# Kernel optimization log

Measured on AMD Instinct MI355X. Metric: run time of the kernel, lower is better.

The kernel has to match this reference:

```python
import jax, jax.numpy as jnp
import numpy as np

ALPHA = 0.2  # LeakyReLU negative slope

def setup_inputs() -> dict:
    key = jax.random.key(0)
    k1, k2, k3, k4 = jax.random.split(key, 4)
    N, F_in, F_out = 8192, 512, 64
    x = jax.random.normal(k1, (N, F_in), dtype=jnp.float32)
    adj = jax.random.randint(k2, (N, N), 0, 2, dtype=jnp.int32)
    # xavier-normal-ish init
    weight = jax.random.normal(k3, (F_in, F_out), dtype=jnp.float32) * np.sqrt(2.0 / (F_in + F_out))
    a = jax.random.normal(k4, (2 * F_out, 1), dtype=jnp.float32) * np.sqrt(2.0 / (2 * F_out + 1))
    return {"x": x, "adj": adj, "weight": weight, "a": a}

def reference(x, adj, weight, a):
    # Wh: [N, F_out]
    Wh = x @ weight
    F_out = weight.shape[1]
    a1 = a[:F_out, 0]   # applies to source (row) node
    a2 = a[F_out:, 0]   # applies to target (col) node
    # e[i,j] = LeakyReLU(Wh[i]@a1 + Wh[j]@a2)  -- broadcast-add instead of O(N^2*2F) concat
    s1 = Wh @ a1        # [N]
    s2 = Wh @ a2        # [N]
    e = s1[:, None] + s2[None, :]              # [N, N]
    e = jnp.where(e > 0, e, ALPHA * e)         # LeakyReLU
    e = jnp.where(adj > 0, e, jnp.float32(-9e15))
    attention = jax.nn.softmax(e, axis=1)      # [N, N]
    h_prime = attention @ Wh                   # [N, F_out]
    return jax.nn.elu(h_prime)                 # concat=True -> ELU
```

## Files before the change

### kernel.cpp

```cpp
#include <hip/hip_runtime.h>
#include <hip/hip_bf16.h>
#include <cstdint>
#include <cstddef>

#define N_NODES 8192
#define F_IN 512
#define F_OUT 64
#define LOG2E 1.44269504f

#define JSPLIT 8
#define JPB (N_NODES / JSPLIT)

typedef __attribute__((ext_vector_type(8))) short short8v;
typedef __attribute__((ext_vector_type(4))) float f32x4;
typedef __attribute__((ext_vector_type(4))) int i32x4;
typedef __attribute__((ext_vector_type(4))) unsigned int u32x4;

static __device__ __forceinline__ unsigned short f2bf(float f) {
    union { float f; unsigned u; } v; v.f = f;
    unsigned u = v.u + 0x7FFFu + ((v.u >> 16) & 1u);
    return (unsigned short)(u >> 16);
}
static __device__ __forceinline__ float bf2f(unsigned short b) {
    union { unsigned u; float f; } v; v.u = ((unsigned)b) << 16;
    return v.f;
}
static __device__ __forceinline__ unsigned cvt_pk_bf16(float lo, float hi) {
    unsigned r;
    asm("v_cvt_pk_bf16_f32 %0, %1, %2" : "=v"(r) : "v"(lo), "v"(hi));
    return r;
}

__global__ __launch_bounds__(256)
void gat_wconv(const float* __restrict__ W, unsigned short* __restrict__ whf,
               unsigned short* __restrict__ wlf) {
    const int t = blockIdx.x * 256 + threadIdx.x;
    const int tile = t >> 6, lane = t & 63;
    const int kt = tile >> 2, ct = tile & 3;
    const int k0 = kt * 32 + ((lane >> 4) << 3);
    const int c  = ct * 16 + (lane & 15);
    short8v h, l;
    #pragma unroll
    for (int i = 0; i < 8; ++i) {
        float v = W[(size_t)(k0 + i) * F_OUT + c];
        unsigned short hb = f2bf(v);
        h[i] = (short)hb;
        l[i] = (short)f2bf(v - bf2f(hb));
    }
    const size_t dst = (size_t)tile * 512 + (size_t)lane * 8;
    *(short8v*)(whf + dst) = h;
    *(short8v*)(wlf + dst) = l;
}

__global__ __launch_bounds__(256)
void gat_prep(const float* __restrict__ x, const unsigned short* __restrict__ whf,
              const unsigned short* __restrict__ wlf, const float* __restrict__ a,
              unsigned short* __restrict__ whtf,
              float* __restrict__ s1, float* __restrict__ s2) {
    __shared__ f32x4 red[2][4][64];
    __shared__ unsigned short ldsT[64][40];
    const int tid = threadIdx.x;
    const int lane = tid & 63;
    const int wv = tid >> 6;
    const int rt = wv & 1;
    const int kh = wv >> 1;
    const int l15 = lane & 15, g = lane >> 4;
    const int jt = blockIdx.x;
    const int row0 = jt * 32 + rt * 16;

    f32x4 acc[4] = {{0.f,0.f,0.f,0.f},{0.f,0.f,0.f,0.f},{0.f,0.f,0.f,0.f},{0.f,0.f,0.f,0.f}};

    const float* xp = x + (size_t)(row0 + l15) * F_IN + kh * 256 + g * 8;
    float4 v[16];
    #pragma unroll
    for (int q = 0; q < 8; ++q) {
        v[2 * q]     = *(const float4*)(xp + q * 32);
        v[2 * q + 1] = *(const float4*)(xp + q * 32 + 4);
    }
    #pragma unroll
    for (int q = 0; q < 8; ++q) {
        const int kt = kh * 8 + q;
        float vv[8] = {v[2*q].x, v[2*q].y, v[2*q].z, v[2*q].w,
                       v[2*q+1].x, v[2*q+1].y, v[2*q+1].z, v[2*q+1].w};
        short8v xh, xl;
        #pragma unroll
        for (int i = 0; i < 8; ++i) {
            unsigned short hb = f2bf(vv[i]);
            xh[i] = (short)hb;
            xl[i] = (short)f2bf(vv[i] - bf2f(hb));
        }
        const unsigned short* wp = whf + (size_t)(kt * 4) * 512 + (size_t)lane * 8;
        const unsigned short* lp = wlf + (size_t)(kt * 4) * 512 + (size_t)lane * 8;
        #pragma unroll
        for (int ct = 0; ct < 4; ++ct) {
            short8v wh = *(const short8v*)(wp + ct * 512);
            short8v wl = *(const short8v*)(lp + ct * 512);
            acc[ct] = __builtin_amdgcn_mfma_f32_16x16x32_bf16(xh, wh, acc[ct], 0, 0, 0);
            acc[ct] = __builtin_amdgcn_mfma_f32_16x16x32_bf16(xl, wh, acc[ct], 0, 0, 0);
            acc[ct] = __builtin_amdgcn_mfma_f32_16x16x32_bf16(xh, wl, acc[ct], 0, 0, 0);
        }
    }

    if (kh == 1) {
        #pragma unroll
        for (int ct = 0; ct < 4; ++ct) red[rt][ct][lane] = acc[ct];
    }
    __syncthreads();

    if (kh == 0) {
        #pragma unroll
        for (int ct = 0; ct < 4; ++ct) acc[ct] += red[rt][ct][lane];

        #pragma unroll
        for (int r = 0; r < 4; ++r) {
            float p1 = 0.f, p2 = 0.f;
            #pragma unroll
            for (int ct = 0; ct < 4; ++ct) {
                p1 = fmaf(acc[ct][r], a[ct * 16 + l15], p1);
                p2 = fmaf(acc[ct][r], a[64 + ct * 16 + l15], p2);
            }
            p1 += __shfl_xor(p1, 1); p2 += __shfl_xor(p2, 1);
            p1 += __shfl_xor(p1, 2); p2 += __shfl_xor(p2, 2);
            p1 += __shfl_xor(p1, 4); p2 += __shfl_xor(p2, 4);
            p1 += __shfl_xor(p1, 8); p2 += __shfl_xor(p2, 8);
            if (l15 == 0) {
                s1[row0 + g * 4 + r] = p1 * LOG2E;
                s2[row0 + g * 4 + r] = p2 * LOG2E;
            }
        }

        #pragma unroll
        for (int ct = 0; ct < 4; ++ct) {
            ushort4 pk;
            pk.x = f2bf(acc[ct][0]); pk.y = f2bf(acc[ct][1]);
            pk.z = f2bf(acc[ct][2]); pk.w = f2bf(acc[ct][3]);
            *(ushort4*)&ldsT[ct * 16 + l15][rt * 16 + g * 4] = pk;
        }
    }
    __syncthreads();

    if (kh == 0) {
        #pragma unroll
        for (int fl = 0; fl < 2; ++fl) {
            const int ft = rt * 2 + fl;
            short8v sv = *(const short8v*)&ldsT[ft * 16 + l15][g * 8];
            *(short8v*)(whtf + ((size_t)jt * 4 + ft) * 512 + (size_t)lane * 8) = sv;
        }
    }
}

__global__ __launch_bounds__(512, 4)
void gat_main(const int* __restrict__ adj, const unsigned short* __restrict__ whtf,
              const float* __restrict__ s1, const float* __restrict__ s2,
              float* __restrict__ numpart, float* __restrict__ denpart) {
    const int tid  = threadIdx.x;
    const int lane = tid & 63;
    const int wv   = tid >> 6;
    const int l15  = lane & 15, g = lane >> 4;
    const int rg   = blockIdx.x >> 3;
    const int js   = blockIdx.x & 7;
    const int rowbase = rg * 128 + wv * 16;
    const int row  = rowbase + l15;
    const int j0   = js * JPB;
    const float s1r = s1[row];

    const int*   aprow = adj + (size_t)row * N_NODES + j0 + g * 8;
    const float* s2b   = s2 + j0 + g * 8;
    const unsigned short* bp = whtf + ((size_t)(j0 >> 5) * 4) * 512 + (size_t)lane * 8;

    f32x4 acc0 = {0.f, 0.f, 0.f, 0.f};
    f32x4 acc1 = acc0, acc2 = acc0, acc3 = acc0;
    float dsum = 0.f;

    for (int grp = 0; grp < JPB / 128; ++grp) {
        i32x4 aj[8];
        #pragma unroll
        for (int q = 0; q < 4; ++q) {
            const i32x4* ap = (const i32x4*)(aprow + grp * 128 + q * 32);
            aj[2 * q]     = ap[0];
            aj[2 * q + 1] = ap[1];
        }
        #pragma unroll
        for (int q = 0; q < 4; ++q) {
            const int jw = grp * 128 + q * 32;
            float4 sa = *(const float4*)(s2b + jw);
            float4 sb = *(const float4*)(s2b + jw + 4);

            const unsigned short* bq = bp + (size_t)(grp * 4 + q) * 2048;
            short8v b0 = *(const short8v*)(bq);
            short8v b1 = *(const short8v*)(bq + 512);
            short8v b2 = *(const short8v*)(bq + 1024);
            short8v b3 = *(const short8v*)(bq + 1536);

            float w0, w1, w2, w3, w4, w5, w6, w7;
            #define GAT_EL(wvar, ajv, s2v) do { \
                float e = s1r + (s2v); e = fmaxf(e, 0.2f * e); \
                float ex = __builtin_amdgcn_exp2f(e); \
                wvar = ((ajv) > 0) ? ex : 0.f; dsum += wvar; } while (0);
            GAT_EL(w0, aj[2*q][0], sa.x) GAT_EL(w1, aj[2*q][1], sa.y)
            GAT_EL(w2, aj[2*q][2], sa.z) GAT_EL(w3, aj[2*q][3], sa.w)
            GAT_EL(w4, aj[2*q+1][0], sb.x) GAT_EL(w5, aj[2*q+1][1], sb.y)
            GAT_EL(w6, aj[2*q+1][2], sb.z) GAT_EL(w7, aj[2*q+1][3], sb.w)
            #undef GAT_EL

            u32x4 au;
            au[0] = cvt_pk_bf16(w0, w1);
            au[1] = cvt_pk_bf16(w2, w3);
            au[2] = cvt_pk_bf16(w4, w5);
            au[3] = cvt_pk_bf16(w6, w7);
            short8v afrag = __builtin_bit_cast(short8v, au);

            acc0 = __builtin_amdgcn_mfma_f32_16x16x32_bf16(afrag, b0, acc0, 0, 0, 0);
            acc1 = __builtin_amdgcn_mfma_f32_16x16x32_bf16(afrag, b1, acc1, 0, 0, 0);
            acc2 = __builtin_amdgcn_mfma_f32_16x16x32_bf16(afrag, b2, acc2, 0, 0, 0);
            acc3 = __builtin_amdgcn_mfma_f32_16x16x32_bf16(afrag, b3, acc3, 0, 0, 0);
        }
    }

    dsum += __shfl_xor(dsum, 16);
    dsum += __shfl_xor(dsum, 32);
    if (lane < 16) denpart[(size_t)js * N_NODES + rowbase + lane] = dsum;

    float* np = numpart + ((size_t)js * N_NODES + rowbase) * F_OUT;
    #pragma unroll
    for (int r = 0; r < 4; ++r) {
        const int ro = (g * 4 + r) * F_OUT;
        np[ro +  0 + l15] = acc0[r];
        np[ro + 16 + l15] = acc1[r];
        np[ro + 32 + l15] = acc2[r];
        np[ro + 48 + l15] = acc3[r];
    }
}

__global__ __launch_bounds__(256)
void gat_combine(const float* __restrict__ numpart, const float* __restrict__ denpart,
                 float* __restrict__ out) {
    const int idx = blockIdx.x * 256 + threadIdx.x;
    const int r = idx >> 6;
    float num = 0.f, den = 0.f;
    #pragma unroll
    for (int c = 0; c < JSPLIT; ++c) {
        num += numpart[(size_t)c * N_NODES * F_OUT + idx];
        den += denpart[(size_t)c * N_NODES + r];
    }
    float h = num / den;
    out[idx] = h > 0.f ? h : __expf(h) - 1.f;
}

extern "C" void kernel_launch(void* const* d_in, const int* in_sizes, int n_in,
                              void* d_out, int out_size, void* d_ws, size_t ws_size,
                              hipStream_t stream) {
    const float* x      = (const float*)d_in[0];
    const int*   adj    = (const int*)d_in[1];
    const float* weight = (const float*)d_in[2];
    const float* a      = (const float*)d_in[3];
    float* out = (float*)d_out;

    char* ws = (char*)d_ws;
    unsigned short* whtf = (unsigned short*)ws;
    float* s1            = (float*)(ws + 1048576);
    float* s2            = (float*)(ws + 1048576 + 32768);
    unsigned short* whf  = (unsigned short*)(ws + 1048576 + 65536);
    unsigned short* wlf  = (unsigned short*)(ws + 1048576 + 131072);
    float* numpart       = (float*)(ws + 1048576 + 196608);
    float* denpart       = (float*)(ws + 1048576 + 196608 + (size_t)JSPLIT * N_NODES * F_OUT * 4);

    gat_wconv<<<16, 256, 0, stream>>>(weight, whf, wlf);
    gat_prep<<<N_NODES / 32, 256, 0, stream>>>(x, whf, wlf, a, whtf, s1, s2);
    gat_main<<<64 * JSPLIT, 512, 0, stream>>>(adj, whtf, s1, s2, numpart, denpart);
    gat_combine<<<N_NODES * F_OUT / 256, 256, 0, stream>>>(numpart, denpart, out);
}
```

Before: 103.0 us.

## Stage Wh slice in LDS and double-buffer adjacency loads in gat_main

Each block now copies its 1024-column slice of the bf16 Wh tile (128KB) into shared memory with global_load_lds before the loop, and reads MFMA B fragments from LDS rather than global memory. The adjacency loads are double-buffered across two register arrays so the next batch's loads are issued while the current one is consumed. The min-blocks hint in launch_bounds is dropped. The 128KB of LDS per block caps occupancy at about one block per CU and raises register pressure, which may cut the latency hiding needed for streaming the adjacency matrix.

```diff
diff --git a/kernel.cpp b/kernel.cpp
--- a/kernel.cpp
+++ b/kernel.cpp
@@ -149,10 +149,11 @@
     }
 }
 
-__global__ __launch_bounds__(512, 4)
+__global__ __launch_bounds__(512)
 void gat_main(const int* __restrict__ adj, const unsigned short* __restrict__ whtf,
               const float* __restrict__ s1, const float* __restrict__ s2,
               float* __restrict__ numpart, float* __restrict__ denpart) {
+    __shared__ unsigned short lds[JPB * F_OUT * 2 / 2];
     const int tid  = threadIdx.x;
     const int lane = tid & 63;
     const int wv   = tid >> 6;
@@ -164,58 +165,88 @@
     const int j0   = js * JPB;
     const float s1r = s1[row];
 
+    {
+        const char* gsrc = (const char*)(whtf + (size_t)(j0 >> 5) * 4 * 512) + (size_t)tid * 16;
+        char* ldst = (char*)&lds[0] + (size_t)tid * 16;
+        #pragma unroll
+        for (int r = 0; r < 16; ++r)
+            __builtin_amdgcn_global_load_lds(
+                (const __attribute__((address_space(1))) void*)(gsrc + r * 8192),
+                (__attribute__((address_space(3))) void*)(ldst + r * 8192), 16, 0, 0);
+    }
+
     const int*   aprow = adj + (size_t)row * N_NODES + j0 + g * 8;
     const float* s2b   = s2 + j0 + g * 8;
-    const unsigned short* bp = whtf + ((size_t)(j0 >> 5) * 4) * 512 + (size_t)lane * 8;
+
+    __syncthreads();
 
     f32x4 acc0 = {0.f, 0.f, 0.f, 0.f};
     f32x4 acc1 = acc0, acc2 = acc0, acc3 = acc0;
     float dsum = 0.f;
 
-    for (int grp = 0; grp < JPB / 128; ++grp) {
-        i32x4 aj[8];
-        #pragma unroll
-        for (int q = 0; q < 4; ++q) {
-            const i32x4* ap = (const i32x4*)(aprow + grp * 128 + q * 32);
-            aj[2 * q]     = ap[0];
-            aj[2 * q + 1] = ap[1];
-        }
-        #pragma unroll
-        for (int q = 0; q < 4; ++q) {
-            const int jw = grp * 128 + q * 32;
-            float4 sa = *(const float4*)(s2b + jw);
-            float4 sb = *(const float4*)(s2b + jw + 4);
-
-            const unsigned short* bq = bp + (size_t)(grp * 4 + q) * 2048;
-            short8v b0 = *(const short8v*)(bq);
-            short8v b1 = *(const short8v*)(bq + 512);
-            short8v b2 = *(const short8v*)(bq + 1024);
-            short8v b3 = *(const short8v*)(bq + 1536);
-
-            float w0, w1, w2, w3, w4, w5, w6, w7;
-            #define GAT_EL(wvar, ajv, s2v) do { \
-                float e = s1r + (s2v); e = fmaxf(e, 0.2f * e); \
-                float ex = __builtin_amdgcn_exp2f(e); \
-                wvar = ((ajv) > 0) ? ex : 0.f; dsum += wvar; } while (0);
-            GAT_EL(w0, aj[2*q][0], sa.x) GAT_EL(w1, aj[2*q][1], sa.y)
-            GAT_EL(w2, aj[2*q][2], sa.z) GAT_EL(w3, aj[2*q][3], sa.w)
-            GAT_EL(w4, aj[2*q+1][0], sb.x) GAT_EL(w5, aj[2*q+1][1], sb.y)
-            GAT_EL(w6, aj[2*q+1][2], sb.z) GAT_EL(w7, aj[2*q+1][3], sb.w)
-            #undef GAT_EL
-
-            u32x4 au;
-            au[0] = cvt_pk_bf16(w0, w1);
-            au[1] = cvt_pk_bf16(w2, w3);
-            au[2] = cvt_pk_bf16(w4, w5);
-            au[3] = cvt_pk_bf16(w6, w7);
-            short8v afrag = __builtin_bit_cast(short8v, au);
-
-            acc0 = __builtin_amdgcn_mfma_f32_16x16x32_bf16(afrag, b0, acc0, 0, 0, 0);
-            acc1 = __builtin_amdgcn_mfma_f32_16x16x32_bf16(afrag, b1, acc1, 0, 0, 0);
-            acc2 = __builtin_amdgcn_mfma_f32_16x16x32_bf16(afrag, b2, acc2, 0, 0, 0);
-            acc3 = __builtin_amdgcn_mfma_f32_16x16x32_bf16(afrag, b3, acc3, 0, 0, 0);
-        }
-    }
+    i32x4 ajA[8], ajB[8];
+
+    #define LOADBATCH(BUF, b) do { \
+        _Pragma("unroll") \
+        for (int _q = 0; _q < 4; ++_q) { \
+            const i32x4* _ap = (const i32x4*)(aprow + (b) * 128 + _q * 32); \
+            BUF[2 * _q]     = _ap[0]; \
+            BUF[2 * _q + 1] = _ap[1]; \
+        } \
+    } while (0)
+
+    #define CONSUME(BUF, b) do { \
+        _Pragma("unroll") \
+        for (int _q = 0; _q < 4; ++_q) { \
+            const int _it = (b) * 4 + _q; \
+            float4 sa = *(const float4*)(s2b + _it * 32); \
+            float4 sb = *(const float4*)(s2b + _it * 32 + 4); \
+            const unsigned short* _gb = &lds[0] + (size_t)_it * 2048 + lane * 8; \
+            short8v b0 = *(const short8v*)(_gb); \
+            short8v b1 = *(const short8v*)(_gb + 512); \
+            short8v b2 = *(const short8v*)(_gb + 1024); \
+            short8v b3 = *(const short8v*)(_gb + 1536); \
+            float w0, w1, w2, w3, w4, w5, w6, w7; \
+            { float e, ex; \
+              e = s1r + sa.x; e = fmaxf(e, 0.2f * e); ex = __builtin_amdgcn_exp2f(e); \
+              w0 = (BUF[2*_q][0] > 0) ? ex : 0.f; dsum += w0; \
+              e = s1r + sa.y; e = fmaxf(e, 0.2f * e); ex = __builtin_amdgcn_exp2f(e); \
+              w1 = (BUF[2*_q][1] > 0) ? ex : 0.f; dsum += w1; \
+              e = s1r + sa.z; e = fmaxf(e, 0.2f * e); ex = __builtin_amdgcn_exp2f(e); \
+              w2 = (BUF[2*_q][2] > 0) ? ex : 0.f; dsum += w2; \
+              e = s1r + sa.w; e = fmaxf(e, 0.2f * e); ex = __builtin_amdgcn_exp2f(e); \
+              w3 = (BUF[2*_q][3] > 0) ? ex : 0.f; dsum += w3; \
+              e = s1r + sb.x; e = fmaxf(e, 0.2f * e); ex = __builtin_amdgcn_exp2f(e); \
+              w4 = (BUF[2*_q+1][0] > 0) ? ex : 0.f; dsum += w4; \
+              e = s1r + sb.y; e = fmaxf(e, 0.2f * e); ex = __builtin_amdgcn_exp2f(e); \
+              w5 = (BUF[2*_q+1][1] > 0) ? ex : 0.f; dsum += w5; \
+              e = s1r + sb.z; e = fmaxf(e, 0.2f * e); ex = __builtin_amdgcn_exp2f(e); \
+              w6 = (BUF[2*_q+1][2] > 0) ? ex : 0.f; dsum += w6; \
+              e = s1r + sb.w; e = fmaxf(e, 0.2f * e); ex = __builtin_amdgcn_exp2f(e); \
+              w7 = (BUF[2*_q+1][3] > 0) ? ex : 0.f; dsum += w7; } \
+            u32x4 au; \
+            au[0] = cvt_pk_bf16(w0, w1); \
+            au[1] = cvt_pk_bf16(w2, w3); \
+            au[2] = cvt_pk_bf16(w4, w5); \
+            au[3] = cvt_pk_bf16(w6, w7); \
+            short8v afrag = __builtin_bit_cast(short8v, au); \
+            acc0 = __builtin_amdgcn_mfma_f32_16x16x32_bf16(afrag, b0, acc0, 0, 0, 0); \
+            acc1 = __builtin_amdgcn_mfma_f32_16x16x32_bf16(afrag, b1, acc1, 0, 0, 0); \
+            acc2 = __builtin_amdgcn_mfma_f32_16x16x32_bf16(afrag, b2, acc2, 0, 0, 0); \
+            acc3 = __builtin_amdgcn_mfma_f32_16x16x32_bf16(afrag, b3, acc3, 0, 0, 0); \
+        } \
+    } while (0)
+
+    LOADBATCH(ajA, 0);
+    #pragma unroll
+    for (int bb = 0; bb < 4; ++bb) {
+        LOADBATCH(ajB, 2 * bb + 1);
+        CONSUME(ajA, 2 * bb);
+        if (bb < 3) LOADBATCH(ajA, 2 * bb + 2);
+        CONSUME(ajB, 2 * bb + 1);
+    }
+    #undef LOADBATCH
+    #undef CONSUME
 
     dsum += __shfl_xor(dsum, 16);
     dsum += __shfl_xor(dsum, 32);
@@ -262,8 +293,8 @@
     float* s2            = (float*)(ws + 1048576 + 32768);
     unsigned short* whf  = (unsigned short*)(ws + 1048576 + 65536);
     unsigned short* wlf  = (unsigned short*)(ws + 1048576 + 131072);
-    float* numpart       = (float*)(ws + 1048576 + 196608);
-    float* denpart       = (float*)(ws + 1048576 + 196608 + (size_t)JSPLIT * N_NODES * F_OUT * 4);
+    float* numpart       = (float*)(ws + 1245184);
+    float* denpart       = (float*)(ws + 1245184 + 16777216);
 
     gat_wconv<<<16, 256, 0, stream>>>(weight, whf, wlf);
     gat_prep<<<N_NODES / 32, 256, 0, stream>>>(x, whf, wlf, a, whtf, s1, s2);
```

After: 97.99 us. 4.9% less time.
